# Kernel tuning notes

Measured on AMD Instinct MI355X. Metric: run time of the kernel, lower is better.

The kernel has to match this reference:

```python
import jax, jax.numpy as jnp
from jax import lax
import numpy as np

L_BANDS = 28
H = 1024
W = 1024


def setup_inputs() -> dict:
    key = jax.random.key(0)
    k1, k2 = jax.random.split(key)
    x_1lhw = jax.random.uniform(k1, (1, L_BANDS, H, W), dtype=jnp.float32)
    mask2d = jax.random.uniform(k2, (H, W), dtype=jnp.float32)
    phi_d_deg = jnp.ones((1,), dtype=jnp.float32)  # dispersion axis angle in degrees
    s_nom = 2.0 * jnp.arange(L_BANDS, dtype=jnp.float32)  # 2 px/band nominal dispersion
    return {"x_1lhw": x_1lhw, "mask2d": mask2d, "phi_d_deg": phi_d_deg, "s_nom": s_nom}


def _int_offsets(phi_d_deg, s_nom):
    # Mirrors torch: offsets come from .item() => detached constants.
    phi = float(np.asarray(phi_d_deg).reshape(())) * np.pi / 180.0
    s = np.asarray(s_nom, dtype=np.float64)
    dx = s * np.cos(phi)
    dy = s * np.sin(phi)
    dx = dx - dx.min()
    dy = dy - dy.min()
    return np.rint(dx).astype(np.int32), np.rint(dy).astype(np.int32)


def reference(x_1lhw, mask2d, phi_d_deg, s_nom):
    _, L, Hh, Ww = x_1lhw.shape
    dx_i, dy_i = _int_offsets(phi_d_deg, s_nom)
    Hp = Hh + int(dy_i.max())
    Wp = Ww + int(dx_i.max())
    bands = mask2d[None, :, :] * x_1lhw[0]  # [L, H, W] coded bands

    def step(y, inp):
        band, oy, ox = inp
        patch = lax.dynamic_slice(y, (oy, ox), (Hh, Ww)) + band
        return lax.dynamic_update_slice(y, patch, (oy, ox)), None

    y0 = jnp.zeros((Hp, Wp), dtype=x_1lhw.dtype)
    y, _ = lax.scan(step, y0, (bands, jnp.asarray(dy_i), jnp.asarray(dx_i)))
    return y[None]  # [1, Hp, Wp]
```

## Files before the change

### kernel.cpp

```cpp
#include <hip/hip_runtime.h>
#include <math.h>

#define NL 28
#define H 1024
#define W 1024
#define HW (H * W)
#define BROW 1152
#define GUARD 64
#define WBANDS 7
#define NBUF 3
#define WREG (NBUF * BROW)
#define NPASS 9

typedef float f2 __attribute__((ext_vector_type(2), aligned(4)));

typedef __attribute__((address_space(1))) const void GV;
typedef __attribute__((address_space(3))) void LV;
__device__ __forceinline__ void gl_lds16(const float* g, float* l) {
    __builtin_amdgcn_global_load_lds((GV*)g, (LV*)l, 16, 0, 0);
}

__global__ __launch_bounds__(256)
void cassi_v11(const float* __restrict__ x, const float* __restrict__ mask,
               const float* __restrict__ phi_deg, const float* __restrict__ s_nom,
               float* __restrict__ out, int out_size)
{
    __shared__ float lds[4 * WREG + 2 * BROW];

    const int tid = threadIdx.x;
    const int lane = tid & 63;
    const int wid = tid >> 6;

    float phi = phi_deg[0] * 0.017453292519943295f;
    float c = cosf(phi), sn = sinf(phi);
    float s = (lane < NL) ? s_nom[lane] : 0.f;
    float dxv = s * c, dyv = s * sn;
    float dxm = (lane < NL) ? dxv : 3.0e38f;
    float dym = (lane < NL) ? dyv : 3.0e38f;
    for (int d = 1; d < 64; d <<= 1) {
        dxm = fminf(dxm, __shfl_xor(dxm, d, 64));
        dym = fminf(dym, __shfl_xor(dym, d, 64));
    }
    int dxi = (lane < NL) ? (int)rintf(dxv - dxm) : 0;
    int dyi = (lane < NL) ? (int)rintf(dyv - dym) : 0;
    int dxmax = dxi, dymax = dyi;
    for (int d = 1; d < 64; d <<= 1) {
        dxmax = max(dxmax, __shfl_xor(dxmax, d, 64));
        dymax = max(dymax, __shfl_xor(dymax, d, 64));
    }
    const int Wp = W + dxmax;
    const int Hp = out_size / Wp;

    if (!(dymax <= 1 && dxmax <= GUARD)) {
        for (int i = blockIdx.x * 256 + tid; i < out_size; i += gridDim.x * 256) {
            int Yk = i / Wp, Xk = i - Yk * Wp;
            float a = 0.f;
            for (int l = 0; l < NL; ++l) {
                float sl = s_nom[l];
                int dx = (int)rintf(sl * c - dxm);
                int dy = (int)rintf(sl * sn - dym);
                int h = Yk - dy, w = Xk - dx;
                if ((unsigned)h < (unsigned)H && (unsigned)w < (unsigned)W) {
                    int p = h * W + w;
                    a = fmaf(mask[p], x[(size_t)l * HW + p], a);
                }
            }
            out[i] = a;
        }
        return;
    }

    const int Y = blockIdx.x;
    if (Y >= Hp) return;

    float* xw = &lds[wid * WREG];
    float* mb = &lds[4 * WREG];

#pragma unroll
    for (int b = 0; b < NBUF; ++b) {
        xw[b * BROW + lane] = 0.f;
        xw[b * BROW + GUARD + 1024 + lane] = 0.f;
    }
    if (wid < 2) {
        int g = Y - wid;
        float* mrow = &mb[wid * BROW];
        if ((unsigned)g < (unsigned)H) {
            const float* src = mask + (size_t)g * W + lane * 4;
            gl_lds16(src,       mrow + GUARD);
            gl_lds16(src + 256, mrow + GUARD + 256);
            gl_lds16(src + 512, mrow + GUARD + 512);
            gl_lds16(src + 768, mrow + GUARD + 768);
            mrow[lane] = 0.f;
            mrow[GUARD + 1024 + lane] = 0.f;
        } else {
            for (int k = lane; k < BROW; k += 64) mrow[k] = 0.f;
        }
    }
#pragma unroll
    for (int j = 0; j < 2; ++j) {
        int l = wid * WBANDS + j;
        int dyj = __shfl(dyi, l, 64);
        int srow = min(max(Y - dyj, 0), H - 1);
        const float* src = x + (size_t)l * HW + (size_t)srow * W + lane * 4;
        float* dst = xw + j * BROW + GUARD;
        gl_lds16(src, dst);
        gl_lds16(src + 256, dst + 256);
        gl_lds16(src + 512, dst + 512);
        gl_lds16(src + 768, dst + 768);
    }
    asm volatile("s_waitcnt vmcnt(8) lgkmcnt(0)" ::: "memory");
    __builtin_amdgcn_s_barrier();

    int te[NPASS];
#pragma unroll
    for (int p = 0; p < NPASS; ++p) {
        int t = p * 128 + 2 * lane;
        te[p] = (t < Wp) ? t : 0;
    }

    f2 acc[NPASS];
#pragma unroll
    for (int p = 0; p < NPASS; ++p) acc[p] = f2{0.f, 0.f};

#pragma unroll
    for (int j = 0; j < WBANDS; ++j) {
        if (j + 2 < WBANDS) {
            int l = wid * WBANDS + j + 2;
            int dyj = __shfl(dyi, l, 64);
            int srow = min(max(Y - dyj, 0), H - 1);
            const float* src = x + (size_t)l * HW + (size_t)srow * W + lane * 4;
            float* dst = xw + ((j + 2) % NBUF) * BROW + GUARD;
            gl_lds16(src, dst);
            gl_lds16(src + 256, dst + 256);
            gl_lds16(src + 512, dst + 512);
            gl_lds16(src + 768, dst + 768);
        }
        if (j + 2 < WBANDS)      asm volatile("s_waitcnt vmcnt(8)" ::: "memory");
        else if (j + 1 < WBANDS) asm volatile("s_waitcnt vmcnt(4)" ::: "memory");
        else                     asm volatile("s_waitcnt vmcnt(0)" ::: "memory");

        int l = wid * WBANDS + j;
        int dxj = __shfl(dxi, l, 64);
        int dyj = __shfl(dyi, l, 64);
        const float* xb = xw + (j % NBUF) * BROW + GUARD - dxj;
        const float* mrow = mb + dyj * BROW + GUARD - dxj;
#pragma unroll
        for (int p = 0; p < NPASS; ++p) {
            f2 xv = *(const f2*)&xb[te[p]];
            f2 mv = *(const f2*)&mrow[te[p]];
            acc[p] += xv * mv;
        }
        asm volatile("s_waitcnt lgkmcnt(0)" ::: "memory");
        __builtin_amdgcn_sched_barrier(0);
    }

#pragma unroll
    for (int p = 0; p < NPASS; ++p) {
        int t = p * 128 + 2 * lane;
        if (t + 1 < Wp)      *(f2*)&xw[t] = acc[p];
        else if (t < Wp)     xw[t] = acc[p].x;
    }
    asm volatile("s_waitcnt lgkmcnt(0)" ::: "memory");
    __builtin_amdgcn_s_barrier();

    float* orow = out + (size_t)Y * Wp;
#pragma unroll
    for (int q = 0; q < 3; ++q) {
        int t = 2 * (tid + q * 256);
        if (t + 1 < Wp) {
            f2 v = *(const f2*)&lds[0 * WREG + t];
            v += *(const f2*)&lds[1 * WREG + t];
            v += *(const f2*)&lds[2 * WREG + t];
            v += *(const f2*)&lds[3 * WREG + t];
            *(f2*)&orow[t] = v;
        } else if (t < Wp) {
            orow[t] = lds[0 * WREG + t] + lds[1 * WREG + t]
                    + lds[2 * WREG + t] + lds[3 * WREG + t];
        }
    }
}

extern "C" void kernel_launch(void* const* d_in, const int* in_sizes, int n_in,
                              void* d_out, int out_size, void* d_ws, size_t ws_size,
                              hipStream_t stream) {
    const float* x = (const float*)d_in[0];
    const float* mask = (const float*)d_in[1];
    const float* phi = (const float*)d_in[2];
    const float* s_nom = (const float*)d_in[3];
    float* out = (float*)d_out;

    const int blocks = out_size / W + 2;
    cassi_v11<<<blocks, 256, 0, stream>>>(x, mask, phi, s_nom, out, out_size);
}
```

Baseline: 28.54 us.

## Use two waves per block with fourteen bands each and precomputed offsets

```diff
diff --git a/kernel.cpp b/kernel.cpp
--- a/kernel.cpp
+++ b/kernel.cpp
@@ -7,7 +7,8 @@
 #define HW (H * W)
 #define BROW 1152
 #define GUARD 64
-#define WBANDS 7
+#define NWAVE 2
+#define WBANDS 14
 #define NBUF 3
 #define WREG (NBUF * BROW)
 #define NPASS 9
@@ -20,12 +21,12 @@
     __builtin_amdgcn_global_load_lds((GV*)g, (LV*)l, 16, 0, 0);
 }
 
-__global__ __launch_bounds__(256)
-void cassi_v11(const float* __restrict__ x, const float* __restrict__ mask,
+__global__ __launch_bounds__(128, 2)
+void cassi_v12(const float* __restrict__ x, const float* __restrict__ mask,
                const float* __restrict__ phi_deg, const float* __restrict__ s_nom,
                float* __restrict__ out, int out_size)
 {
-    __shared__ float lds[4 * WREG + 2 * BROW];
+    __shared__ float lds[NWAVE * WREG + 2 * BROW];
 
     const int tid = threadIdx.x;
     const int lane = tid & 63;
@@ -52,7 +53,7 @@
     const int Hp = out_size / Wp;
 
     if (!(dymax <= 1 && dxmax <= GUARD)) {
-        for (int i = blockIdx.x * 256 + tid; i < out_size; i += gridDim.x * 256) {
+        for (int i = blockIdx.x * 128 + tid; i < out_size; i += gridDim.x * 128) {
             int Yk = i / Wp, Xk = i - Yk * Wp;
             float a = 0.f;
             for (int l = 0; l < NL; ++l) {
@@ -74,14 +75,25 @@
     if (Y >= Hp) return;
 
     float* xw = &lds[wid * WREG];
-    float* mb = &lds[4 * WREG];
+    float* mb = &lds[NWAVE * WREG];
+
+    int xo_[WBANDS], mo_[WBANDS], sr_[WBANDS];
+#pragma unroll
+    for (int j = 0; j < WBANDS; ++j) {
+        int l = wid * WBANDS + j;
+        int dxj = __shfl(dxi, l, 64);
+        int dyj = __shfl(dyi, l, 64);
+        xo_[j] = (j % NBUF) * BROW + GUARD - dxj;
+        mo_[j] = dyj * BROW + GUARD - dxj;
+        sr_[j] = min(max(Y - dyj, 0), H - 1);
+    }
 
 #pragma unroll
     for (int b = 0; b < NBUF; ++b) {
         xw[b * BROW + lane] = 0.f;
         xw[b * BROW + GUARD + 1024 + lane] = 0.f;
     }
-    if (wid < 2) {
+    {
         int g = Y - wid;
         float* mrow = &mb[wid * BROW];
         if ((unsigned)g < (unsigned)H) {
@@ -99,9 +111,7 @@
 #pragma unroll
     for (int j = 0; j < 2; ++j) {
         int l = wid * WBANDS + j;
-        int dyj = __shfl(dyi, l, 64);
-        int srow = min(max(Y - dyj, 0), H - 1);
-        const float* src = x + (size_t)l * HW + (size_t)srow * W + lane * 4;
+        const float* src = x + (size_t)l * HW + (size_t)sr_[j] * W + lane * 4;
         float* dst = xw + j * BROW + GUARD;
         gl_lds16(src, dst);
         gl_lds16(src + 256, dst + 256);
@@ -126,9 +136,7 @@
     for (int j = 0; j < WBANDS; ++j) {
         if (j + 2 < WBANDS) {
             int l = wid * WBANDS + j + 2;
-            int dyj = __shfl(dyi, l, 64);
-            int srow = min(max(Y - dyj, 0), H - 1);
-            const float* src = x + (size_t)l * HW + (size_t)srow * W + lane * 4;
+            const float* src = x + (size_t)l * HW + (size_t)sr_[j + 2] * W + lane * 4;
             float* dst = xw + ((j + 2) % NBUF) * BROW + GUARD;
             gl_lds16(src, dst);
             gl_lds16(src + 256, dst + 256);
@@ -139,11 +147,8 @@
         else if (j + 1 < WBANDS) asm volatile("s_waitcnt vmcnt(4)" ::: "memory");
         else                     asm volatile("s_waitcnt vmcnt(0)" ::: "memory");
 
-        int l = wid * WBANDS + j;
-        int dxj = __shfl(dxi, l, 64);
-        int dyj = __shfl(dyi, l, 64);
-        const float* xb = xw + (j % NBUF) * BROW + GUARD - dxj;
-        const float* mrow = mb + dyj * BROW + GUARD - dxj;
+        const float* xb = xw + xo_[j];
+        const float* mrow = mb + mo_[j];
 #pragma unroll
         for (int p = 0; p < NPASS; ++p) {
             f2 xv = *(const f2*)&xb[te[p]];
@@ -157,25 +162,21 @@
 #pragma unroll
     for (int p = 0; p < NPASS; ++p) {
         int t = p * 128 + 2 * lane;
-        if (t + 1 < Wp)      *(f2*)&xw[t] = acc[p];
-        else if (t < Wp)     xw[t] = acc[p].x;
+        *(f2*)&xw[t] = acc[p];
     }
     asm volatile("s_waitcnt lgkmcnt(0)" ::: "memory");
     __builtin_amdgcn_s_barrier();
 
     float* orow = out + (size_t)Y * Wp;
 #pragma unroll
-    for (int q = 0; q < 3; ++q) {
-        int t = 2 * (tid + q * 256);
+    for (int q = 0; q < 5; ++q) {
+        int t = 2 * (tid + q * 128);
         if (t + 1 < Wp) {
-            f2 v = *(const f2*)&lds[0 * WREG + t];
-            v += *(const f2*)&lds[1 * WREG + t];
-            v += *(const f2*)&lds[2 * WREG + t];
-            v += *(const f2*)&lds[3 * WREG + t];
+            f2 v = *(const f2*)&lds[t];
+            v += *(const f2*)&lds[WREG + t];
             *(f2*)&orow[t] = v;
         } else if (t < Wp) {
-            orow[t] = lds[0 * WREG + t] + lds[1 * WREG + t]
-                    + lds[2 * WREG + t] + lds[3 * WREG + t];
+            orow[t] = lds[t] + lds[WREG + t];
         }
     }
 }
@@ -190,5 +191,5 @@
     float* out = (float*)d_out;
 
     const int blocks = out_size / W + 2;
-    cassi_v11<<<blocks, 256, 0, stream>>>(x, mask, phi, s_nom, out, out_size);
+    cassi_v12<<<blocks, 128, 0, stream>>>(x, mask, phi, s_nom, out, out_size);
 }
```

After: 26.96 us. 1.06x faster.

## Use single-wave blocks processing all bands per row, dropping LDS cross-wave reduction

Applied to the files above, without the earlier changes.

```diff
diff --git a/kernel.cpp b/kernel.cpp
--- a/kernel.cpp
+++ b/kernel.cpp
@@ -7,9 +7,7 @@
 #define HW (H * W)
 #define BROW 1152
 #define GUARD 64
-#define WBANDS 7
 #define NBUF 3
-#define WREG (NBUF * BROW)
 #define NPASS 9
 
 typedef float f2 __attribute__((ext_vector_type(2), aligned(4)));
@@ -20,16 +18,14 @@
     __builtin_amdgcn_global_load_lds((GV*)g, (LV*)l, 16, 0, 0);
 }
 
-__global__ __launch_bounds__(256)
-void cassi_v11(const float* __restrict__ x, const float* __restrict__ mask,
+__global__ __launch_bounds__(64)
+void cassi_v14(const float* __restrict__ x, const float* __restrict__ mask,
                const float* __restrict__ phi_deg, const float* __restrict__ s_nom,
                float* __restrict__ out, int out_size)
 {
-    __shared__ float lds[4 * WREG + 2 * BROW];
+    __shared__ float lds[(NBUF + 2) * BROW];
 
-    const int tid = threadIdx.x;
-    const int lane = tid & 63;
-    const int wid = tid >> 6;
+    const int lane = threadIdx.x;
 
     float phi = phi_deg[0] * 0.017453292519943295f;
     float c = cosf(phi), sn = sinf(phi);
@@ -52,7 +48,7 @@
     const int Hp = out_size / Wp;
 
     if (!(dymax <= 1 && dxmax <= GUARD)) {
-        for (int i = blockIdx.x * 256 + tid; i < out_size; i += gridDim.x * 256) {
+        for (int i = blockIdx.x * 64 + lane; i < out_size; i += gridDim.x * 64) {
             int Yk = i / Wp, Xk = i - Yk * Wp;
             float a = 0.f;
             for (int l = 0; l < NL; ++l) {
@@ -73,17 +69,13 @@
     const int Y = blockIdx.x;
     if (Y >= Hp) return;
 
-    float* xw = &lds[wid * WREG];
-    float* mb = &lds[4 * WREG];
+    float* xw = lds;
+    float* mb = lds + NBUF * BROW;
 
 #pragma unroll
-    for (int b = 0; b < NBUF; ++b) {
-        xw[b * BROW + lane] = 0.f;
-        xw[b * BROW + GUARD + 1024 + lane] = 0.f;
-    }
-    if (wid < 2) {
-        int g = Y - wid;
-        float* mrow = &mb[wid * BROW];
+    for (int r = 0; r < 2; ++r) {
+        int g = Y - r;
+        float* mrow = mb + r * BROW;
         if ((unsigned)g < (unsigned)H) {
             const float* src = mask + (size_t)g * W + lane * 4;
             gl_lds16(src,       mrow + GUARD);
@@ -97,19 +89,21 @@
         }
     }
 #pragma unroll
+    for (int b = 0; b < NBUF; ++b) {
+        xw[b * BROW + lane] = 0.f;
+        xw[b * BROW + GUARD + 1024 + lane] = 0.f;
+    }
+#pragma unroll
     for (int j = 0; j < 2; ++j) {
-        int l = wid * WBANDS + j;
-        int dyj = __shfl(dyi, l, 64);
+        int dyj = __shfl(dyi, j, 64);
         int srow = min(max(Y - dyj, 0), H - 1);
-        const float* src = x + (size_t)l * HW + (size_t)srow * W + lane * 4;
+        const float* src = x + (size_t)j * HW + (size_t)srow * W + lane * 4;
         float* dst = xw + j * BROW + GUARD;
         gl_lds16(src, dst);
         gl_lds16(src + 256, dst + 256);
         gl_lds16(src + 512, dst + 512);
         gl_lds16(src + 768, dst + 768);
     }
-    asm volatile("s_waitcnt vmcnt(8) lgkmcnt(0)" ::: "memory");
-    __builtin_amdgcn_s_barrier();
 
     int te[NPASS];
 #pragma unroll
@@ -117,15 +111,14 @@
         int t = p * 128 + 2 * lane;
         te[p] = (t < Wp) ? t : 0;
     }
-
     f2 acc[NPASS];
 #pragma unroll
     for (int p = 0; p < NPASS; ++p) acc[p] = f2{0.f, 0.f};
 
 #pragma unroll
-    for (int j = 0; j < WBANDS; ++j) {
-        if (j + 2 < WBANDS) {
-            int l = wid * WBANDS + j + 2;
+    for (int j = 0; j < NL; ++j) {
+        if (j + 2 < NL) {
+            int l = j + 2;
             int dyj = __shfl(dyi, l, 64);
             int srow = min(max(Y - dyj, 0), H - 1);
             const float* src = x + (size_t)l * HW + (size_t)srow * W + lane * 4;
@@ -135,13 +128,12 @@
             gl_lds16(src + 512, dst + 512);
             gl_lds16(src + 768, dst + 768);
         }
-        if (j + 2 < WBANDS)      asm volatile("s_waitcnt vmcnt(8)" ::: "memory");
-        else if (j + 1 < WBANDS) asm volatile("s_waitcnt vmcnt(4)" ::: "memory");
-        else                     asm volatile("s_waitcnt vmcnt(0)" ::: "memory");
+        if (j + 2 < NL)      asm volatile("s_waitcnt vmcnt(8)" ::: "memory");
+        else if (j + 1 < NL) asm volatile("s_waitcnt vmcnt(4)" ::: "memory");
+        else                 asm volatile("s_waitcnt vmcnt(0)" ::: "memory");
 
-        int l = wid * WBANDS + j;
-        int dxj = __shfl(dxi, l, 64);
-        int dyj = __shfl(dyi, l, 64);
+        int dxj = __shfl(dxi, j, 64);
+        int dyj = __shfl(dyi, j, 64);
         const float* xb = xw + (j % NBUF) * BROW + GUARD - dxj;
         const float* mrow = mb + dyj * BROW + GUARD - dxj;
 #pragma unroll
@@ -154,29 +146,12 @@
         __builtin_amdgcn_sched_barrier(0);
     }
 
+    float* orow = out + (size_t)Y * Wp;
 #pragma unroll
     for (int p = 0; p < NPASS; ++p) {
         int t = p * 128 + 2 * lane;
-        if (t + 1 < Wp)      *(f2*)&xw[t] = acc[p];
-        else if (t < Wp)     xw[t] = acc[p].x;
-    }
-    asm volatile("s_waitcnt lgkmcnt(0)" ::: "memory");
-    __builtin_amdgcn_s_barrier();
-
-    float* orow = out + (size_t)Y * Wp;
-#pragma unroll
-    for (int q = 0; q < 3; ++q) {
-        int t = 2 * (tid + q * 256);
-        if (t + 1 < Wp) {
-            f2 v = *(const f2*)&lds[0 * WREG + t];
-            v += *(const f2*)&lds[1 * WREG + t];
-            v += *(const f2*)&lds[2 * WREG + t];
-            v += *(const f2*)&lds[3 * WREG + t];
-            *(f2*)&orow[t] = v;
-        } else if (t < Wp) {
-            orow[t] = lds[0 * WREG + t] + lds[1 * WREG + t]
-                    + lds[2 * WREG + t] + lds[3 * WREG + t];
-        }
+        if (t + 1 < Wp)  *(f2*)&orow[t] = acc[p];
+        else if (t < Wp) orow[t] = acc[p].x;
     }
 }
 
@@ -190,5 +165,5 @@
     float* out = (float*)d_out;
 
     const int blocks = out_size / W + 2;
-    cassi_v11<<<blocks, 256, 0, stream>>>(x, mask, phi, s_nom, out, out_size);
+    cassi_v14<<<blocks, 64, 0, stream>>>(x, mask, phi, s_nom, out, out_size);
 }
```

New measurement: 101.8 us. +256.8%, slower.
